# Kernel optimization log

Hardware: AMD Instinct MI355X
Metric: run time of the kernel (lower is better)

The kernel has to match this reference:

```python
import jax, jax.numpy as jnp
import numpy as np

N_NODES = 100000
N_EDGES = 1000000
IN_DIM = 128
OUT_DIM = 64
NEG_SLOPE = 0.2


def setup_inputs() -> dict:
    key = jax.random.key(0)
    k = jax.random.split(key, 6)
    h = jax.random.normal(k[0], (N_NODES, IN_DIM), dtype=jnp.float32)
    # xavier-uniform-ish scales for linear weights
    W_w = jax.random.uniform(k[1], (OUT_DIM, IN_DIM), dtype=jnp.float32,
                             minval=-1.0, maxval=1.0) * np.sqrt(6.0 / (IN_DIM + OUT_DIM))
    W_b = jnp.zeros((OUT_DIM,), dtype=jnp.float32)
    a_w = jax.random.uniform(k[2], (1, 2 * OUT_DIM), dtype=jnp.float32,
                             minval=-1.0, maxval=1.0) * np.sqrt(6.0 / (2 * OUT_DIM + 1))
    a_b = jnp.zeros((1,), dtype=jnp.float32)
    edge_index = jax.random.randint(k[3], (2, N_EDGES), 0, N_NODES, dtype=jnp.int64)
    return {"h": h, "W_w": W_w, "W_b": W_b, "a_w": a_w, "a_b": a_b,
            "edge_index": edge_index}


def reference(h, W_w, W_b, a_w, a_b, edge_index):
    # Wh = W(h): [N, D_out]
    Wh = h @ W_w.T + W_b
    src, tgt = edge_index[0], edge_index[1]
    D = Wh.shape[1]
    # a([e_src, e_tgt]) decomposes: score = Wh@a_src per-node + Wh@a_tgt per-node,
    # gathered by edge (avoids materializing the [E, 2D] concat).
    s_src = Wh @ a_w[0, :D]   # [N]
    s_tgt = Wh @ a_w[0, D:]   # [N]
    logits = jax.nn.leaky_relu(s_src[src] + s_tgt[tgt] + a_b[0], NEG_SLOPE)  # [E]
    # NOTE: global softmax over all edges (dim=0), faithful to the source.
    attn = jax.nn.softmax(logits, axis=0)
    e_src = Wh[src]  # [E, D] gather
    messages = jnp.zeros_like(Wh).at[tgt].add(attn[:, None] * e_src)  # scatter-add
    return jax.nn.leaky_relu(messages, NEG_SLOPE)
```

## Files before the change

kernel.cpp:

```cpp
#include <hip/hip_runtime.h>
#include <math.h>

#define N_NODES 100000
#define N_EDGES 1000000
#define IN_DIM  128
#define OUT_DIM 64
#define NEG     0.2f

#define SCAN_BLOCKS 391
#define EDGE_BLOCKS 3907

#define G_GROUPS 80
#define EPG      (N_EDGES / G_GROUPS)
#define NI2      (EPG / 2)
#define CHUNK_N  25000
#define HIST_BLOCKS (G_GROUPS * 4)

typedef __attribute__((ext_vector_type(8))) short short8;
typedef __attribute__((ext_vector_type(4))) float f32x4;

#define MFMA(A, B, C) __builtin_amdgcn_mfma_f32_16x16x32_bf16(A, B, C, 0, 0, 0)

union U16 { unsigned u[4]; short8 s; };

__device__ __forceinline__ void split8(const float* x, short8& hi, short8& lo) {
    U16 H, L;
#pragma unroll
    for (int i = 0; i < 4; ++i) {
        float a = x[2 * i], b = x[2 * i + 1];
        unsigned ua = __float_as_uint(a), ub = __float_as_uint(b);
        unsigned ha = ua & 0xffff0000u, hb = ub & 0xffff0000u;
        H.u[i] = (ua >> 16) | hb;
        float la = a - __uint_as_float(ha);
        float lb = b - __uint_as_float(hb);
        L.u[i] = (__float_as_uint(la) >> 16) | (__float_as_uint(lb) & 0xffff0000u);
    }
    hi = H.s; lo = L.s;
}

__device__ __forceinline__ unsigned pk2(float a, float b) {
    unsigned ua = __float_as_uint(a); ua = (ua + 0x7fffu + ((ua >> 16) & 1u)) >> 16;
    unsigned ub = __float_as_uint(b); ub = (ub + 0x7fffu + ((ub >> 16) & 1u)) >> 16;
    return ua | (ub << 16);
}

__global__ __launch_bounds__(256, 3) void k1_mfma(
    const float* __restrict__ h, const float* __restrict__ W,
    const float* __restrict__ Wb, const float* __restrict__ aw,
    unsigned short* __restrict__ Whb, float* __restrict__ s_src,
    float* __restrict__ s_tgt)
{
    __shared__ float4 smem4[2176];
    unsigned short* wfh = (unsigned short*)smem4;
    unsigned short* wfl = wfh + 8192;

    const int tid  = threadIdx.x;
    const int lane = tid & 63, w = tid >> 6;
    const int c = lane & 15, g = lane >> 4;
    const int n0 = blockIdx.x * 128;

#pragma unroll
    for (int it = 0; it < 4; ++it) {
        int U = tid + 256 * it;
        int pos = U >> 6, l = U & 63;
        int nb = pos >> 2, ks = pos & 3;
        int r  = 16 * nb + (l & 15);
        int k0 = 32 * ks + 8 * (l >> 4);
        float a[8];
        *(float4*)&a[0] = *(const float4*)(W + r * IN_DIM + k0);
        *(float4*)&a[4] = *(const float4*)(W + r * IN_DIM + k0 + 4);
        short8 hi, lo; split8(a, hi, lo);
        *(short8*)(wfh + (size_t)U * 8) = hi;
        *(short8*)(wfl + (size_t)U * 8) = lo;
    }
    __syncthreads();

    const int na0 = n0 + 32 * w + c;
    const float* hp0 = h + (size_t)min(na0, N_NODES - 1) * IN_DIM + 8 * g;
    const float* hp1 = h + (size_t)min(na0 + 16, N_NODES - 1) * IN_DIM + 8 * g;

    f32x4 acc[2][4];
    {
        f32x4 z = {0.f, 0.f, 0.f, 0.f};
#pragma unroll
        for (int m = 0; m < 2; ++m)
#pragma unroll
            for (int nb = 0; nb < 4; ++nb) acc[m][nb] = z;
    }

#pragma unroll 2
    for (int ks = 0; ks < 4; ++ks) {
        short8 bh[4], bl[4];
#pragma unroll
        for (int nb = 0; nb < 4; ++nb) {
            int u = ((nb * 4 + ks) * 64 + lane) * 8;
            bh[nb] = *(const short8*)(wfh + u);
            bl[nb] = *(const short8*)(wfl + u);
        }
        float am[8];
        short8 ah, al;
        *(float4*)&am[0] = *(const float4*)(hp0 + 32 * ks);
        *(float4*)&am[4] = *(const float4*)(hp0 + 32 * ks + 4);
        split8(am, ah, al);
#pragma unroll
        for (int nb = 0; nb < 4; ++nb) {
            acc[0][nb] = MFMA(ah, bh[nb], acc[0][nb]);
            acc[0][nb] = MFMA(ah, bl[nb], acc[0][nb]);
            acc[0][nb] = MFMA(al, bh[nb], acc[0][nb]);
        }
        *(float4*)&am[0] = *(const float4*)(hp1 + 32 * ks);
        *(float4*)&am[4] = *(const float4*)(hp1 + 32 * ks + 4);
        split8(am, ah, al);
#pragma unroll
        for (int nb = 0; nb < 4; ++nb) {
            acc[1][nb] = MFMA(ah, bh[nb], acc[1][nb]);
            acc[1][nb] = MFMA(ah, bl[nb], acc[1][nb]);
            acc[1][nb] = MFMA(al, bh[nb], acc[1][nb]);
        }
    }

    float wb[4], w1[4], w2[4];
#pragma unroll
    for (int nb = 0; nb < 4; ++nb) {
        wb[nb] = Wb[16 * nb + c];
        w1[nb] = aw[16 * nb + c];
        w2[nb] = aw[OUT_DIM + 16 * nb + c];
    }
#pragma unroll
    for (int m = 0; m < 2; ++m)
#pragma unroll
        for (int r = 0; r < 4; ++r) {
            float s1 = 0.f, s2 = 0.f;
#pragma unroll
            for (int nb = 0; nb < 4; ++nb) {
                float v = acc[m][nb][r] + wb[nb];
                acc[m][nb][r] = v;
                s1 = fmaf(v, w1[nb], s1);
                s2 = fmaf(v, w2[nb], s2);
            }
#pragma unroll
            for (int mk = 1; mk < 16; mk <<= 1) {
                s1 += __shfl_xor(s1, mk);
                s2 += __shfl_xor(s2, mk);
            }
            if (c == 0) {
                int node = n0 + 32 * w + 16 * m + 4 * g + r;
                if (node < N_NODES) { s_src[node] = s1; s_tgt[node] = s2; }
            }
        }

    __syncthreads();
    float* tr = (float*)smem4;
#pragma unroll
    for (int m = 0; m < 2; ++m)
#pragma unroll
        for (int nb = 0; nb < 4; ++nb)
#pragma unroll
            for (int r = 0; r < 4; ++r)
                tr[(32 * w + 16 * m + 4 * g + r) * 68 + 16 * nb + c] = acc[m][nb][r];
    __syncthreads();

#pragma unroll
    for (int j = 0; j < 4; ++j) {
        int idx = tid + 256 * j;
        int nloc = idx >> 3, q = idx & 7;
        int node = n0 + nloc;
        if (node < N_NODES) {
            const float* r8 = &tr[nloc * 68 + q * 8];
            uint4 u;
            u.x = pk2(r8[0], r8[1]); u.y = pk2(r8[2], r8[3]);
            u.z = pk2(r8[4], r8[5]); u.w = pk2(r8[6], r8[7]);
            ((uint4*)Whb)[(size_t)node * 8 + q] = u;
        }
    }
}

__global__ __launch_bounds__(256) void k_hist(
    const int* __restrict__ ei, unsigned char* __restrict__ deg_g8,
    unsigned* __restrict__ rank)
{
    __shared__ unsigned cnt[CHUNK_N / 2];
    const int g  = blockIdx.x >> 2;
    const int c0 = (blockIdx.x & 3) * CHUNK_N;
    const int tid = threadIdx.x;

    for (int i = tid; i < CHUNK_N / 2; i += 256) cnt[i] = 0u;
    __syncthreads();

    const int ebase = g * EPG;
    const int2* tp2 = (const int2*)(ei + N_EDGES + ebase);
    for (int b = 0; b < 32; b += 8) {
        int2 tv[8];
#pragma unroll
        for (int k = 0; k < 8; ++k) {
            int idx = tid + (b + k) * 256;
            tv[k] = (idx < NI2) ? tp2[idx] : make_int2(-0x40000000, -0x40000000);
        }
#pragma unroll
        for (int k = 0; k < 8; ++k) {
            int idx = tid + (b + k) * 256;
            int e0 = ebase + 2 * idx;
            unsigned u0 = (unsigned)(tv[k].x - c0), u1 = (unsigned)(tv[k].y - c0);
            if (u0 < CHUNK_N) {
                unsigned sh = (u0 & 1u) * 16u;
                unsigned old = atomicAdd(&cnt[u0 >> 1], 1u << sh);
                rank[e0] = (old >> sh) & 0xffffu;
            }
            if (u1 < CHUNK_N) {
                unsigned sh = (u1 & 1u) * 16u;
                unsigned old = atomicAdd(&cnt[u1 >> 1], 1u << sh);
                rank[e0 + 1] = (old >> sh) & 0xffffu;
            }
        }
    }
    __syncthreads();

    unsigned* dg = (unsigned*)(deg_g8 + (size_t)g * N_NODES + c0);
    for (int i = tid; i < CHUNK_N / 4; i += 256) {
        unsigned w0 = cnt[2 * i], w1 = cnt[2 * i + 1];
        dg[i] = (w0 & 0xffu) | (((w0 >> 16) & 0xffu) << 8) |
                ((w1 & 0xffu) << 16) | (((w1 >> 16) & 0xffu) << 24);
    }
}

__global__ __launch_bounds__(256) void k_scanA(
    const unsigned char* __restrict__ deg_g8, unsigned* __restrict__ psum)
{
    const int i = blockIdx.x * 256 + threadIdx.x;
    unsigned v = 0;
    if (i < N_NODES) {
#pragma unroll
        for (int x = 0; x < G_GROUPS; ++x)
            v += deg_g8[(size_t)x * N_NODES + i];
    }
#pragma unroll
    for (int off = 32; off; off >>= 1) v += __shfl_xor(v, off);
    __shared__ unsigned us[4];
    if ((threadIdx.x & 63) == 0) us[threadIdx.x >> 6] = v;
    __syncthreads();
    if (threadIdx.x == 0) psum[blockIdx.x] = us[0] + us[1] + us[2] + us[3];
}

__global__ __launch_bounds__(256) void k_scan3(
    const unsigned char* __restrict__ deg_g8, const unsigned* __restrict__ psum,
    unsigned* __restrict__ row, unsigned* __restrict__ row_g)
{
    __shared__ unsigned sc[256];
    __shared__ unsigned ps[4];
    const int t = threadIdx.x;
    const int i = blockIdx.x * 256 + t;

    unsigned pv = 0;
    if (t < blockIdx.x) pv = psum[t];
    if (t + 256 < blockIdx.x) pv += psum[t + 256];
#pragma unroll
    for (int off = 32; off; off >>= 1) pv += __shfl_xor(pv, off);
    if ((t & 63) == 0) ps[t >> 6] = pv;

    unsigned tot = 0;
    if (i < N_NODES) {
#pragma unroll
        for (int x = 0; x < G_GROUPS; ++x)
            tot += deg_g8[(size_t)x * N_NODES + i];
    }
    sc[t] = tot;
    __syncthreads();
    for (int off = 1; off < 256; off <<= 1) {
        unsigned u = (t >= off) ? sc[t - off] : 0u;
        __syncthreads();
        sc[t] += u;
        __syncthreads();
    }
    const unsigned bb = ps[0] + ps[1] + ps[2] + ps[3];
    if (i < N_NODES) {
        unsigned base = bb + sc[t] - tot;
        row[i] = base;
        unsigned run = base;
#pragma unroll
        for (int x = 0; x < G_GROUPS; ++x) {
            row_g[(size_t)x * N_NODES + i] = run;
            run += deg_g8[(size_t)x * N_NODES + i];
        }
    }
    if (i == 0) row[N_NODES] = N_EDGES;
}

__global__ __launch_bounds__(256) void k_fill(
    const int* __restrict__ ei, const float* __restrict__ s_src,
    const float* __restrict__ s_tgt, const float* __restrict__ ab,
    const unsigned* __restrict__ rank, const unsigned* __restrict__ row_g,
    int2* __restrict__ bin, float* __restrict__ bsum)
{
    const float ab0 = ab[0];
    float lsum = 0.f;
    const int e = blockIdx.x * 256 + threadIdx.x;
    if (e < N_EDGES) {
        int s = ei[e], t = ei[N_EDGES + e];
        float x = s_src[s] + s_tgt[t] + ab0;
        float l = x > 0.f ? x : NEG * x;
        float ex = __expf(l);
        lsum = ex;
        int g = e / EPG;
        unsigned pos = row_g[(size_t)g * N_NODES + t] + rank[e];
        bin[pos] = make_int2(s, __float_as_int(ex));
    }
#pragma unroll
    for (int off = 32; off; off >>= 1) lsum += __shfl_xor(lsum, off);
    __shared__ float ssum[4];
    if ((threadIdx.x & 63) == 0) ssum[threadIdx.x >> 6] = lsum;
    __syncthreads();
    if (threadIdx.x == 0)
        bsum[blockIdx.x] = ssum[0] + ssum[1] + ssum[2] + ssum[3];
}

__global__ __launch_bounds__(512) void k_gsum(
    const float* __restrict__ bsum, float* __restrict__ gsum)
{
    __shared__ float sf[8];
    const int t = threadIdx.x;
    float s = 0.f;
    for (int i = t; i < EDGE_BLOCKS; i += 512) s += bsum[i];
#pragma unroll
    for (int off = 32; off; off >>= 1) s += __shfl_xor(s, off);
    if ((t & 63) == 0) sf[t >> 6] = s;
    __syncthreads();
    if (t == 0) {
        float tot = 0.f;
#pragma unroll
        for (int i = 0; i < 8; ++i) tot += sf[i];
        gsum[0] = tot;
    }
}

__global__ __launch_bounds__(256) void k_gather(
    const unsigned* __restrict__ row, const int2* __restrict__ bin,
    const float* __restrict__ gsum, const unsigned short* __restrict__ Whb,
    float* __restrict__ out)
{
    const int lane = threadIdx.x & 63;
    const int tb = blockIdx.x * 16 + (threadIdx.x >> 6) * 4;
    const int q = lane >> 4, sub = lane & 15;

    const unsigned r0 = row[tb],     r1 = row[tb + 1], r2 = row[tb + 2];
    const unsigned r3 = row[tb + 3], r4 = row[tb + 4];
    unsigned base0 = r0, base1 = r1, base2 = r2, base3 = r3;

    f32x4 a0 = {0.f, 0.f, 0.f, 0.f}, a1 = a0, a2 = a0, a3 = a0;

    while (base0 < r1 || base1 < r2 || base2 < r3 || base3 < r4) {
        const int c0 = base0 < r1 ? (int)min(64u, r1 - base0) : 0;
        const int c1 = base1 < r2 ? (int)min(64u, r2 - base1) : 0;
        const int c2 = base2 < r3 ? (int)min(64u, r3 - base2) : 0;
        const int c3 = base3 < r4 ? (int)min(64u, r4 - base3) : 0;
        int2 p0 = make_int2(0, 0), p1 = p0, p2 = p0, p3 = p0;
        if (lane < c0) p0 = bin[base0 + lane];
        if (lane < c1) p1 = bin[base1 + lane];
        if (lane < c2) p2 = bin[base2 + lane];
        if (lane < c3) p3 = bin[base3 + lane];
        const int cm = max(max(c0, c1), max(c2, c3));
        for (int j = 0; j < cm; j += 4) {
            int   s0 = __shfl(p0.x, j + q);
            float w0 = __int_as_float(__shfl(p0.y, j + q));
            int   s1 = __shfl(p1.x, j + q);
            float w1 = __int_as_float(__shfl(p1.y, j + q));
            int   s2 = __shfl(p2.x, j + q);
            float w2 = __int_as_float(__shfl(p2.y, j + q));
            int   s3 = __shfl(p3.x, j + q);
            float w3 = __int_as_float(__shfl(p3.y, j + q));
            ushort4 v0 = *(const ushort4*)(Whb + (size_t)s0 * OUT_DIM + 4 * sub);
            ushort4 v1 = *(const ushort4*)(Whb + (size_t)s1 * OUT_DIM + 4 * sub);
            ushort4 v2 = *(const ushort4*)(Whb + (size_t)s2 * OUT_DIM + 4 * sub);
            ushort4 v3 = *(const ushort4*)(Whb + (size_t)s3 * OUT_DIM + 4 * sub);
            a0.x = fmaf(w0, __uint_as_float((unsigned)v0.x << 16), a0.x);
            a0.y = fmaf(w0, __uint_as_float((unsigned)v0.y << 16), a0.y);
            a0.z = fmaf(w0, __uint_as_float((unsigned)v0.z << 16), a0.z);
            a0.w = fmaf(w0, __uint_as_float((unsigned)v0.w << 16), a0.w);
            a1.x = fmaf(w1, __uint_as_float((unsigned)v1.x << 16), a1.x);
            a1.y = fmaf(w1, __uint_as_float((unsigned)v1.y << 16), a1.y);
            a1.z = fmaf(w1, __uint_as_float((unsigned)v1.z << 16), a1.z);
            a1.w = fmaf(w1, __uint_as_float((unsigned)v1.w << 16), a1.w);
            a2.x = fmaf(w2, __uint_as_float((unsigned)v2.x << 16), a2.x);
            a2.y = fmaf(w2, __uint_as_float((unsigned)v2.y << 16), a2.y);
            a2.z = fmaf(w2, __uint_as_float((unsigned)v2.z << 16), a2.z);
            a2.w = fmaf(w2, __uint_as_float((unsigned)v2.w << 16), a2.w);
            a3.x = fmaf(w3, __uint_as_float((unsigned)v3.x << 16), a3.x);
            a3.y = fmaf(w3, __uint_as_float((unsigned)v3.y << 16), a3.y);
            a3.z = fmaf(w3, __uint_as_float((unsigned)v3.z << 16), a3.z);
            a3.w = fmaf(w3, __uint_as_float((unsigned)v3.w << 16), a3.w);
        }
        base0 += 64; base1 += 64; base2 += 64; base3 += 64;
    }

    const float inv = 1.0f / gsum[0];
#pragma unroll
    for (int n = 0; n < 4; ++n) {
        f32x4 a = (n == 0) ? a0 : (n == 1) ? a1 : (n == 2) ? a2 : a3;
        a.x += __shfl_xor(a.x, 16); a.x += __shfl_xor(a.x, 32);
        a.y += __shfl_xor(a.y, 16); a.y += __shfl_xor(a.y, 32);
        a.z += __shfl_xor(a.z, 16); a.z += __shfl_xor(a.z, 32);
        a.w += __shfl_xor(a.w, 16); a.w += __shfl_xor(a.w, 32);
        float r = (q == 0) ? a.x : (q == 1) ? a.y : (q == 2) ? a.z : a.w;
        r *= inv;
        r = r > 0.f ? r : NEG * r;
        out[(size_t)(tb + n) * OUT_DIM + 4 * sub + q] = r;
    }
}

extern "C" void kernel_launch(void* const* d_in, const int* in_sizes, int n_in,
                              void* d_out, int out_size, void* d_ws, size_t ws_size,
                              hipStream_t stream)
{
    const float* h  = (const float*)d_in[0];
    const float* W  = (const float*)d_in[1];
    const float* Wb = (const float*)d_in[2];
    const float* aw = (const float*)d_in[3];
    const float* ab = (const float*)d_in[4];
    const int*   ei = (const int*)d_in[5];

    unsigned short* Whb = (unsigned short*)d_ws;
    int2*  bin   = (int2*)(Whb + (size_t)N_NODES * OUT_DIM);
    float* s_src = (float*)(bin + N_EDGES);
    float* s_tgt = s_src + N_NODES;
    unsigned char* deg_g8 = (unsigned char*)(s_tgt + N_NODES);
    unsigned* row   = (unsigned*)(deg_g8 + (size_t)G_GROUPS * N_NODES);
    unsigned* row_g = row + N_NODES + 1;
    unsigned* psum  = row_g + (size_t)G_GROUPS * N_NODES;
    unsigned* rank  = psum + 512;
    float* bsum  = (float*)(rank + N_EDGES);
    float* gsum  = bsum + 4096;

    float* out = (float*)d_out;

    k_hist<<<HIST_BLOCKS, 256, 0, stream>>>(ei, deg_g8, rank);
    k1_mfma<<<(N_NODES + 127) / 128, 256, 0, stream>>>(h, W, Wb, aw, Whb,
                                                       s_src, s_tgt);
    k_scanA<<<SCAN_BLOCKS, 256, 0, stream>>>(deg_g8, psum);
    k_scan3<<<SCAN_BLOCKS, 256, 0, stream>>>(deg_g8, psum, row, row_g);
    k_fill<<<EDGE_BLOCKS, 256, 0, stream>>>(ei, s_src, s_tgt, ab, rank,
                                            row_g, bin, bsum);
    k_gsum<<<1, 512, 0, stream>>>(bsum, gsum);
    k_gather<<<(N_NODES + 15) / 16, 256, 0, stream>>>(row, bin, gsum, Whb, out);
}
```

Measured before the change: 203.0 us.

## Compress per-group row offsets to bytes and process four edges per thread

The per-group absolute row offsets (80 x N unsigned) become 8-bit offsets relative to each node's row start, so the scan writes and fill reads a quarter of the bytes. The fill kernel now handles four edges per thread with all loads batched up front, which raises memory-level parallelism and cuts the block count. The byte offset assumes no node has more than 255 incoming edges before a given group; with random edges the in-degree stays far below that, but a skewed graph would overflow silently.

```diff
diff --git a/kernel.cpp b/kernel.cpp
--- a/kernel.cpp
+++ b/kernel.cpp
@@ -8,7 +8,7 @@
 #define NEG     0.2f
 
 #define SCAN_BLOCKS 391
-#define EDGE_BLOCKS 3907
+#define FILL_BLOCKS 977
 
 #define G_GROUPS 80
 #define EPG      (N_EDGES / G_GROUPS)
@@ -243,7 +243,7 @@
 
 __global__ __launch_bounds__(256) void k_scan3(
     const unsigned char* __restrict__ deg_g8, const unsigned* __restrict__ psum,
-    unsigned* __restrict__ row, unsigned* __restrict__ row_g)
+    unsigned* __restrict__ row, unsigned char* __restrict__ roff)
 {
     __shared__ unsigned sc[256];
     __shared__ unsigned ps[4];
@@ -273,12 +273,11 @@
     }
     const unsigned bb = ps[0] + ps[1] + ps[2] + ps[3];
     if (i < N_NODES) {
-        unsigned base = bb + sc[t] - tot;
-        row[i] = base;
-        unsigned run = base;
+        row[i] = bb + sc[t] - tot;
+        unsigned run = 0;
 #pragma unroll
         for (int x = 0; x < G_GROUPS; ++x) {
-            row_g[(size_t)x * N_NODES + i] = run;
+            roff[(size_t)x * N_NODES + i] = (unsigned char)run;
             run += deg_g8[(size_t)x * N_NODES + i];
         }
     }
@@ -288,21 +287,45 @@
 __global__ __launch_bounds__(256) void k_fill(
     const int* __restrict__ ei, const float* __restrict__ s_src,
     const float* __restrict__ s_tgt, const float* __restrict__ ab,
-    const unsigned* __restrict__ rank, const unsigned* __restrict__ row_g,
+    const unsigned* __restrict__ rank, const unsigned* __restrict__ row,
+    const unsigned char* __restrict__ roff,
     int2* __restrict__ bin, float* __restrict__ bsum)
 {
     const float ab0 = ab[0];
+    const int base = blockIdx.x * 1024 + threadIdx.x;
+
+    int  s[4], t[4], ee[4];
+    bool ok[4];
+#pragma unroll
+    for (int k = 0; k < 4; ++k) {
+        int e = base + 256 * k;
+        ok[k] = e < N_EDGES;
+        ee[k] = ok[k] ? e : 0;
+        s[k] = ei[ee[k]];
+        t[k] = ei[N_EDGES + ee[k]];
+    }
+
+    float xs[4], xt[4];
+    unsigned ps_[4], rk[4];
+#pragma unroll
+    for (int k = 0; k < 4; ++k) {
+        xs[k] = s_src[s[k]];
+        xt[k] = s_tgt[t[k]];
+        int g = ee[k] / EPG;
+        ps_[k] = row[t[k]] + roff[(size_t)g * N_NODES + t[k]];
+        rk[k] = rank[ee[k]];
+    }
+
     float lsum = 0.f;
-    const int e = blockIdx.x * 256 + threadIdx.x;
-    if (e < N_EDGES) {
-        int s = ei[e], t = ei[N_EDGES + e];
-        float x = s_src[s] + s_tgt[t] + ab0;
+#pragma unroll
+    for (int k = 0; k < 4; ++k) {
+        float x = xs[k] + xt[k] + ab0;
         float l = x > 0.f ? x : NEG * x;
         float ex = __expf(l);
-        lsum = ex;
-        int g = e / EPG;
-        unsigned pos = row_g[(size_t)g * N_NODES + t] + rank[e];
-        bin[pos] = make_int2(s, __float_as_int(ex));
+        if (ok[k]) {
+            lsum += ex;
+            bin[ps_[k] + rk[k]] = make_int2(s[k], __float_as_int(ex));
+        }
     }
 #pragma unroll
     for (int off = 32; off; off >>= 1) lsum += __shfl_xor(lsum, off);
@@ -319,7 +342,7 @@
     __shared__ float sf[8];
     const int t = threadIdx.x;
     float s = 0.f;
-    for (int i = t; i < EDGE_BLOCKS; i += 512) s += bsum[i];
+    for (int i = t; i < FILL_BLOCKS; i += 512) s += bsum[i];
 #pragma unroll
     for (int off = 32; off; off >>= 1) s += __shfl_xor(s, off);
     if ((t & 63) == 0) sf[t >> 6] = s;
@@ -422,12 +445,12 @@
     float* s_src = (float*)(bin + N_EDGES);
     float* s_tgt = s_src + N_NODES;
     unsigned char* deg_g8 = (unsigned char*)(s_tgt + N_NODES);
-    unsigned* row   = (unsigned*)(deg_g8 + (size_t)G_GROUPS * N_NODES);
-    unsigned* row_g = row + N_NODES + 1;
-    unsigned* psum  = row_g + (size_t)G_GROUPS * N_NODES;
-    unsigned* rank  = psum + 512;
-    float* bsum  = (float*)(rank + N_EDGES);
-    float* gsum  = bsum + 4096;
+    unsigned* row  = (unsigned*)(deg_g8 + (size_t)G_GROUPS * N_NODES);
+    unsigned char* roff = (unsigned char*)(row + N_NODES + 1);
+    unsigned* psum = (unsigned*)(roff + (size_t)G_GROUPS * N_NODES);
+    unsigned* rank = psum + 512;
+    float* bsum = (float*)(rank + N_EDGES);
+    float* gsum = bsum + 1024;
 
     float* out = (float*)d_out;
 
@@ -435,9 +458,9 @@
     k1_mfma<<<(N_NODES + 127) / 128, 256, 0, stream>>>(h, W, Wb, aw, Whb,
                                                        s_src, s_tgt);
     k_scanA<<<SCAN_BLOCKS, 256, 0, stream>>>(deg_g8, psum);
-    k_scan3<<<SCAN_BLOCKS, 256, 0, stream>>>(deg_g8, psum, row, row_g);
-    k_fill<<<EDGE_BLOCKS, 256, 0, stream>>>(ei, s_src, s_tgt, ab, rank,
-                                            row_g, bin, bsum);
+    k_scan3<<<SCAN_BLOCKS, 256, 0, stream>>>(deg_g8, psum, row, roff);
+    k_fill<<<FILL_BLOCKS, 256, 0, stream>>>(ei, s_src, s_tgt, ab, rank,
+                                            row, roff, bin, bsum);
     k_gsum<<<1, 512, 0, stream>>>(bsum, gsum);
     k_gather<<<(N_NODES + 15) / 16, 256, 0, stream>>>(row, bin, gsum, Whb, out);
 }
```

Measured after the change: 196.3 us (median of 2 runs). 3.3% less time.
